# Optimization experiments

Measured on AMD Instinct MI355X. Metric: run time of the kernel, lower is better.

The kernel has to match this reference:

```python
import jax, jax.numpy as jnp
import numpy as np

ALL_OFFSETS = np.array([1, 3, 4, 13, 15, 21, 23, 28, 48, 64, 96, 192, 384, 512, 768, 1024], dtype=np.int32)
NEG_BIG = -1e30  # finite stand-in for -inf (avoids nan grads)


def setup_inputs() -> dict:
    key = jax.random.key(0)
    k0, k1, k2, k3, k4 = jax.random.split(key, 5)
    B, H, N, HD = 1, 16, 4096, 64
    return {
        "q": jax.random.normal(k0, (B, H, N, HD), dtype=jnp.float32),
        "k": jax.random.normal(k1, (B, H, N, HD), dtype=jnp.float32),
        "v": jax.random.normal(k2, (B, H, N, HD), dtype=jnp.float32),
        "pos_bias": jax.random.normal(k3, (16, H), dtype=jnp.float32) * 0.1,
        "scale_embed": jax.random.normal(k4, (16, HD), dtype=jnp.float32) * 0.1,
    }


def reference(q, k, v, pos_bias, scale_embed):
    # q,k,v: [B,H,N,HD]; pos_bias: [16,H]; scale_embed: [16,HD]
    B, H, N, HD = q.shape
    sc = 1.0 / np.sqrt(HD).astype(np.float32)
    offs = jnp.asarray(ALL_OFFSETS)                      # [16]
    idx = jnp.arange(N)[None, :] - offs[:, None]         # [16,N] key position n-delta
    valid = idx >= 0                                     # [16,N]
    idx_c = jnp.maximum(idx, 0)

    kg = k[:, :, idx_c, :]                               # [B,H,16,N,HD] gathered keys
    vg = v[:, :, idx_c, :]                               # [B,H,16,N,HD] gathered values

    # score = q.k/sqrt(HD) + pos_bias[i,h] + q.se_i/sqrt(HD)
    s = jnp.einsum('bhnd,bhind->bhin', q, kg) * sc
    s = s + pos_bias.T[None, :, :, None]                 # [H,16] -> broadcast over b,n
    s = s + jnp.einsum('bhnd,id->bhin', q, scale_embed) * sc
    s = jnp.where(valid[None, None], s, NEG_BIG)         # [B,H,16,N]

    # stable softmax over the 16 offsets; rows with no valid offset (n=0) yield 0 output
    m = jnp.max(s, axis=2, keepdims=True)                # [B,H,1,N]
    p = jnp.where(valid[None, None], jnp.exp(s - m), 0.0)  # [B,H,16,N]
    l = jnp.sum(p, axis=2)                               # [B,H,N]
    out = jnp.einsum('bhin,bhind->bhnd', p, vg)
    out = out / jnp.where(l > 0.0, l, 1.0)[..., None]
    return out
```

## Files before the change

kernel.cpp:

```cpp
#include <hip/hip_runtime.h>
#include <hip/hip_fp16.h>

typedef __attribute__((address_space(3))) float* lds_f32p;
typedef const __attribute__((address_space(1))) float* glob_f32p;

template<int CTRL>
__device__ __forceinline__ float dpp_add_step(float x) {
    const int p = __builtin_amdgcn_update_dpp(
        0, __builtin_bit_cast(int, x), CTRL, 0xf, 0xf, true);
    return x + __builtin_bit_cast(float, p);
}

__device__ __forceinline__ float dpp_reduce16(float a) {
    a = dpp_add_step<0xB1>(a);
    a = dpp_add_step<0x4E>(a);
    a = dpp_add_step<0x141>(a);
    a = dpp_add_step<0x140>(a);
    return a;
}

__device__ __forceinline__ float4 lds_h4(const __half* p) {
    const __half2* hp = (const __half2*)p;
    const float2 lo = __half22float2(hp[0]);
    const float2 hi = __half22float2(hp[1]);
    return make_float4(lo.x, lo.y, hi.x, hi.y);
}

template<bool SAFE>
__device__ __forceinline__ void run_block(
    const float* __restrict__ kh, const float* __restrict__ vh,
    const float* se_sh, const float* pb2,
    const __half* ksh, const __half* vsh,
    const float4 qa, const float4 qb, const int n0, const int n1,
    const int g, const int jo,
    float4& oa, float4& ob, float& la, float& lb)
{
    constexpr int NEARO[8] = {1, 3, 4, 13, 15, 21, 23, 28};
    constexpr int FARO[8]  = {48, 64, 96, 192, 384, 512, 768, 1024};
    constexpr float SC = 0.125f * 1.44269504f;

#pragma unroll
    for (int t = 0; t < 8; ++t) {
        {
            const int off = FARO[t];
            const int i = t + 8;
            const int ia = n0 - off, ib = n1 - off;
            const int iac = SAFE ? (ia < 0 ? 0 : ia) : ia;
            const int ibc = SAFE ? (ib < 0 ? 0 : ib) : ib;
            const float4 sv = *(const float4*)&se_sh[(i << 6) + jo];
            const float4 ka = *(const float4*)(kh + ((size_t)iac << 6) + jo);
            const float4 kb = *(const float4*)(kh + ((size_t)ibc << 6) + jo);
            const float4 va = *(const float4*)(vh + ((size_t)iac << 6) + jo);
            const float4 vb = *(const float4*)(vh + ((size_t)ibc << 6) + jo);
            float accA = qa.x*(ka.x+sv.x) + qa.y*(ka.y+sv.y) + qa.z*(ka.z+sv.z) + qa.w*(ka.w+sv.w);
            float accB = qb.x*(kb.x+sv.x) + qb.y*(kb.y+sv.y) + qb.z*(kb.z+sv.z) + qb.w*(kb.w+sv.w);
            accA = dpp_reduce16(accA);
            accB = dpp_reduce16(accB);
            float pA = exp2f(fmaf(accA, SC, pb2[i]));
            float pB = exp2f(fmaf(accB, SC, pb2[i]));
            if (SAFE) {
                pA = (ia >= 0) ? pA : 0.f;
                pB = (ib >= 0) ? pB : 0.f;
            }
            la += pA; lb += pB;
            oa.x += pA*va.x; oa.y += pA*va.y; oa.z += pA*va.z; oa.w += pA*va.w;
            ob.x += pB*vb.x; ob.y += pB*vb.y; ob.z += pB*vb.z; ob.w += pB*vb.w;
        }
        {
            const int off = NEARO[t];
            const int i = t;
            const int ia = n0 - off, ib = n1 - off;
            const float4 sv = *(const float4*)&se_sh[(i << 6) + jo];
            const float4 ka = lds_h4(&ksh[((g + 32 - off) << 6) + jo]);
            const float4 kb = lds_h4(&ksh[((g + 48 - off) << 6) + jo]);
            const float4 va = lds_h4(&vsh[((g + 32 - off) << 6) + jo]);
            const float4 vb = lds_h4(&vsh[((g + 48 - off) << 6) + jo]);
            float accA = qa.x*(ka.x+sv.x) + qa.y*(ka.y+sv.y) + qa.z*(ka.z+sv.z) + qa.w*(ka.w+sv.w);
            float accB = qb.x*(kb.x+sv.x) + qb.y*(kb.y+sv.y) + qb.z*(kb.z+sv.z) + qb.w*(kb.w+sv.w);
            accA = dpp_reduce16(accA);
            accB = dpp_reduce16(accB);
            float pA = exp2f(fmaf(accA, SC, pb2[i]));
            float pB = exp2f(fmaf(accB, SC, pb2[i]));
            if (SAFE) {
                pA = (ia >= 0) ? pA : 0.f;
                pB = (ib >= 0) ? pB : 0.f;
            }
            la += pA; lb += pB;
            oa.x += pA*va.x; oa.y += pA*va.y; oa.z += pA*va.z; oa.w += pA*va.w;
            ob.x += pB*vb.x; ob.y += pB*vb.y; ob.z += pB*vb.z; ob.w += pB*vb.w;
        }
    }
}

__global__ __launch_bounds__(256) void dsqg_attn_kernel(
    const float* __restrict__ q, const float* __restrict__ k,
    const float* __restrict__ v, const float* __restrict__ pb,
    const float* __restrict__ se, float* __restrict__ out)
{
    __shared__ __half ksh[64 * 64];
    __shared__ __half vsh[64 * 64];
    __shared__ float se_sh[16 * 64];

    const int p   = blockIdx.x;
    const int lb_ = ((p & 7) << 8) + (p >> 3);
    const int h   = lb_ >> 7;
    const int nb  = lb_ & 127;
    const int base = nb << 5;

    const int g  = threadIdx.x >> 4;
    const int j  = threadIdx.x & 15;
    const int n0 = base + g;
    const int n1 = n0 + 16;
    const size_t hb = (size_t)h << 18;
    const int jo = j << 2;

    const float* kh = k + hb;
    const float* vh = v + hb;

    {
        const float* src = se + (threadIdx.x << 2);
        float* dstbase = &se_sh[(threadIdx.x >> 6) << 8];
        __builtin_amdgcn_global_load_lds((glob_f32p)src, (lds_f32p)dstbase, 16, 0, 0);
    }

    const float4 qa = *(const float4*)(q + hb + ((size_t)n0 << 6) + jo);
    const float4 qb = *(const float4*)(q + hb + ((size_t)n1 << 6) + jo);

    {
        const int wave = threadIdx.x >> 6;
        const int lane = threadIdx.x & 63;
        const int srow = lane >> 4;
        const int scol = (lane & 15) << 2;
#pragma unroll
        for (int i = 0; i < 4; ++i) {
            const int sr = (wave << 4) + (i << 2) + srow;
            int gr = base - 32 + sr;
            gr = gr < 0 ? 0 : gr;
            const size_t go = ((size_t)gr << 6) + scol;
            const float4 kf = *(const float4*)(kh + go);
            const float4 vf = *(const float4*)(vh + go);
            union { __half2 h2[2]; uint2 u; } pk, pv;
            pk.h2[0] = __floats2half2_rn(kf.x, kf.y);
            pk.h2[1] = __floats2half2_rn(kf.z, kf.w);
            pv.h2[0] = __floats2half2_rn(vf.x, vf.y);
            pv.h2[1] = __floats2half2_rn(vf.z, vf.w);
            *(uint2*)&ksh[(sr << 6) + scol] = pk.u;
            *(uint2*)&vsh[(sr << 6) + scol] = pv.u;
        }
    }

    float pb2[16];
#pragma unroll
    for (int i = 0; i < 16; ++i) pb2[i] = pb[(i << 4) + h] * 1.44269504f;

    __syncthreads();

    float la = 0.f, lb2 = 0.f;
    float4 oa = make_float4(0.f, 0.f, 0.f, 0.f);
    float4 ob = make_float4(0.f, 0.f, 0.f, 0.f);

    if (nb >= 32) {
        run_block<false>(kh, vh, se_sh, pb2, ksh, vsh, qa, qb, n0, n1, g, jo, oa, ob, la, lb2);
    } else {
        run_block<true>(kh, vh, se_sh, pb2, ksh, vsh, qa, qb, n0, n1, g, jo, oa, ob, la, lb2);
    }

    const float inva = (la > 0.f) ? 1.f / la : 0.f;
    const float invb = 1.f / lb2;
    oa.x *= inva; oa.y *= inva; oa.z *= inva; oa.w *= inva;
    ob.x *= invb; ob.y *= invb; ob.z *= invb; ob.w *= invb;
    *(float4*)(out + hb + ((size_t)n0 << 6) + jo) = oa;
    *(float4*)(out + hb + ((size_t)n1 << 6) + jo) = ob;
}

extern "C" void kernel_launch(void* const* d_in, const int* in_sizes, int n_in,
                              void* d_out, int out_size, void* d_ws, size_t ws_size,
                              hipStream_t stream) {
    const float* q  = (const float*)d_in[0];
    const float* k  = (const float*)d_in[1];
    const float* v  = (const float*)d_in[2];
    const float* pb = (const float*)d_in[3];
    const float* se = (const float*)d_in[4];
    float* out = (float*)d_out;

    dim3 grid(2048);
    dim3 block(256);
    dsqg_attn_kernel<<<grid, block, 0, stream>>>(q, k, v, pb, se, out);
}
```

Before: 25.38 us.

## Remap threads to 8 lanes per query and precompute scale-embed bias terms

Each query row is now handled by 8 lanes holding 8 dims each, instead of 16 lanes handling two rows with 4 dims each. This shortens the cross-lane DPP reduction to 3 steps and allows 128-bit LDS and global loads. The q·scale_embed term is hoisted out of the per-offset loop into 16 precomputed per-row biases, which removes the add of se to k inside the inner loop. Scale_embed is now staged through LDS as fp16 via a plain register copy instead of global_load_lds, which slightly reduces the precision of the bias.

Result: no change. 24.93 us (-1.8%).

```diff
diff --git a/kernel.cpp b/kernel.cpp
--- a/kernel.cpp
+++ b/kernel.cpp
@@ -1,8 +1,5 @@
 #include <hip/hip_runtime.h>
 #include <hip/hip_fp16.h>
-
-typedef __attribute__((address_space(3))) float* lds_f32p;
-typedef const __attribute__((address_space(1))) float* glob_f32p;
 
 template<int CTRL>
 __device__ __forceinline__ float dpp_add_step(float x) {
@@ -11,29 +8,36 @@
     return x + __builtin_bit_cast(float, p);
 }
 
-__device__ __forceinline__ float dpp_reduce16(float a) {
+__device__ __forceinline__ float dpp_reduce8(float a) {
     a = dpp_add_step<0xB1>(a);
     a = dpp_add_step<0x4E>(a);
     a = dpp_add_step<0x141>(a);
-    a = dpp_add_step<0x140>(a);
     return a;
 }
 
-__device__ __forceinline__ float4 lds_h4(const __half* p) {
-    const __half2* hp = (const __half2*)p;
-    const float2 lo = __half22float2(hp[0]);
-    const float2 hi = __half22float2(hp[1]);
-    return make_float4(lo.x, lo.y, hi.x, hi.y);
+__device__ __forceinline__ void lds_h8(const __half* p, float4& a, float4& b) {
+    const uint4 u = *(const uint4*)p;
+    const float2 f0 = __half22float2(__builtin_bit_cast(__half2, u.x));
+    const float2 f1 = __half22float2(__builtin_bit_cast(__half2, u.y));
+    const float2 f2 = __half22float2(__builtin_bit_cast(__half2, u.z));
+    const float2 f3 = __half22float2(__builtin_bit_cast(__half2, u.w));
+    a = make_float4(f0.x, f0.y, f1.x, f1.y);
+    b = make_float4(f2.x, f2.y, f3.x, f3.y);
+}
+
+__device__ __forceinline__ float dot8(const float4 q0, const float4 q1,
+                                      const float4 a, const float4 b) {
+    return q0.x*a.x + q0.y*a.y + q0.z*a.z + q0.w*a.w
+         + q1.x*b.x + q1.y*b.y + q1.z*b.z + q1.w*b.w;
 }
 
 template<bool SAFE>
 __device__ __forceinline__ void run_block(
     const float* __restrict__ kh, const float* __restrict__ vh,
-    const float* se_sh, const float* pb2,
+    const float* bias,
     const __half* ksh, const __half* vsh,
-    const float4 qa, const float4 qb, const int n0, const int n1,
-    const int g, const int jo,
-    float4& oa, float4& ob, float& la, float& lb)
+    const float4 q0, const float4 q1, const int n, const int ql, const int d8,
+    float4& o0, float4& o1, float& l)
 {
     constexpr int NEARO[8] = {1, 3, 4, 13, 15, 21, 23, 28};
     constexpr int FARO[8]  = {48, 64, 96, 192, 384, 512, 768, 1024};
@@ -42,52 +46,34 @@
 #pragma unroll
     for (int t = 0; t < 8; ++t) {
         {
-            const int off = FARO[t];
-            const int i = t + 8;
-            const int ia = n0 - off, ib = n1 - off;
-            const int iac = SAFE ? (ia < 0 ? 0 : ia) : ia;
-            const int ibc = SAFE ? (ib < 0 ? 0 : ib) : ib;
-            const float4 sv = *(const float4*)&se_sh[(i << 6) + jo];
-            const float4 ka = *(const float4*)(kh + ((size_t)iac << 6) + jo);
-            const float4 kb = *(const float4*)(kh + ((size_t)ibc << 6) + jo);
-            const float4 va = *(const float4*)(vh + ((size_t)iac << 6) + jo);
-            const float4 vb = *(const float4*)(vh + ((size_t)ibc << 6) + jo);
-            float accA = qa.x*(ka.x+sv.x) + qa.y*(ka.y+sv.y) + qa.z*(ka.z+sv.z) + qa.w*(ka.w+sv.w);
-            float accB = qb.x*(kb.x+sv.x) + qb.y*(kb.y+sv.y) + qb.z*(kb.z+sv.z) + qb.w*(kb.w+sv.w);
-            accA = dpp_reduce16(accA);
-            accB = dpp_reduce16(accB);
-            float pA = exp2f(fmaf(accA, SC, pb2[i]));
-            float pB = exp2f(fmaf(accB, SC, pb2[i]));
-            if (SAFE) {
-                pA = (ia >= 0) ? pA : 0.f;
-                pB = (ib >= 0) ? pB : 0.f;
-            }
-            la += pA; lb += pB;
-            oa.x += pA*va.x; oa.y += pA*va.y; oa.z += pA*va.z; oa.w += pA*va.w;
-            ob.x += pB*vb.x; ob.y += pB*vb.y; ob.z += pB*vb.z; ob.w += pB*vb.w;
+            const int off  = FARO[t];
+            const int idx  = n - off;
+            const int idxc = SAFE ? (idx < 0 ? 0 : idx) : idx;
+            const float4* kp = (const float4*)(kh + ((size_t)idxc << 6) + d8);
+            const float4 k0 = kp[0], k1 = kp[1];
+            const float4* vp = (const float4*)(vh + ((size_t)idxc << 6) + d8);
+            const float4 v0 = vp[0], v1 = vp[1];
+            float a = dot8(q0, q1, k0, k1);
+            a = dpp_reduce8(a);
+            float pw = exp2f(fmaf(a, SC, bias[t + 8]));
+            if (SAFE) pw = (idx >= 0) ? pw : 0.f;
+            l += pw;
+            o0.x += pw*v0.x; o0.y += pw*v0.y; o0.z += pw*v0.z; o0.w += pw*v0.w;
+            o1.x += pw*v1.x; o1.y += pw*v1.y; o1.z += pw*v1.z; o1.w += pw*v1.w;
         }
         {
             const int off = NEARO[t];
-            const int i = t;
-            const int ia = n0 - off, ib = n1 - off;
-            const float4 sv = *(const float4*)&se_sh[(i << 6) + jo];
-            const float4 ka = lds_h4(&ksh[((g + 32 - off) << 6) + jo]);
-            const float4 kb = lds_h4(&ksh[((g + 48 - off) << 6) + jo]);
-            const float4 va = lds_h4(&vsh[((g + 32 - off) << 6) + jo]);
-            const float4 vb = lds_h4(&vsh[((g + 48 - off) << 6) + jo]);
-            float accA = qa.x*(ka.x+sv.x) + qa.y*(ka.y+sv.y) + qa.z*(ka.z+sv.z) + qa.w*(ka.w+sv.w);
-            float accB = qb.x*(kb.x+sv.x) + qb.y*(kb.y+sv.y) + qb.z*(kb.z+sv.z) + qb.w*(kb.w+sv.w);
-            accA = dpp_reduce16(accA);
-            accB = dpp_reduce16(accB);
-            float pA = exp2f(fmaf(accA, SC, pb2[i]));
-            float pB = exp2f(fmaf(accB, SC, pb2[i]));
-            if (SAFE) {
-                pA = (ia >= 0) ? pA : 0.f;
-                pB = (ib >= 0) ? pB : 0.f;
-            }
-            la += pA; lb += pB;
-            oa.x += pA*va.x; oa.y += pA*va.y; oa.z += pA*va.z; oa.w += pA*va.w;
-            ob.x += pB*vb.x; ob.y += pB*vb.y; ob.z += pB*vb.z; ob.w += pB*vb.w;
+            const int row = ql + 32 - off;
+            float4 k0, k1, v0, v1;
+            lds_h8(&ksh[(row << 6) + d8], k0, k1);
+            lds_h8(&vsh[(row << 6) + d8], v0, v1);
+            float a = dot8(q0, q1, k0, k1);
+            a = dpp_reduce8(a);
+            float pw = exp2f(fmaf(a, SC, bias[t]));
+            if (SAFE) pw = (n - off >= 0) ? pw : 0.f;
+            l += pw;
+            o0.x += pw*v0.x; o0.y += pw*v0.y; o0.z += pw*v0.z; o0.w += pw*v0.w;
+            o1.x += pw*v1.x; o1.y += pw*v1.y; o1.z += pw*v1.z; o1.w += pw*v1.w;
         }
     }
 }
@@ -99,7 +85,7 @@
 {
     __shared__ __half ksh[64 * 64];
     __shared__ __half vsh[64 * 64];
-    __shared__ float se_sh[16 * 64];
+    __shared__ __half se_sh[16 * 64];
 
     const int p   = blockIdx.x;
     const int lb_ = ((p & 7) << 8) + (p >> 3);
@@ -107,24 +93,19 @@
     const int nb  = lb_ & 127;
     const int base = nb << 5;
 
-    const int g  = threadIdx.x >> 4;
-    const int j  = threadIdx.x & 15;
-    const int n0 = base + g;
-    const int n1 = n0 + 16;
+    const int g   = threadIdx.x >> 4;
+    const int j   = threadIdx.x & 15;
+    const int sub = j >> 3;
+    const int d8  = (j & 7) << 3;
+    const int ql  = (g << 1) + sub;
+    const int n   = base + ql;
     const size_t hb = (size_t)h << 18;
-    const int jo = j << 2;
 
     const float* kh = k + hb;
     const float* vh = v + hb;
 
-    {
-        const float* src = se + (threadIdx.x << 2);
-        float* dstbase = &se_sh[(threadIdx.x >> 6) << 8];
-        __builtin_amdgcn_global_load_lds((glob_f32p)src, (lds_f32p)dstbase, 16, 0, 0);
-    }
-
-    const float4 qa = *(const float4*)(q + hb + ((size_t)n0 << 6) + jo);
-    const float4 qb = *(const float4*)(q + hb + ((size_t)n1 << 6) + jo);
+    const float4* qp = (const float4*)(q + hb + ((size_t)n << 6) + d8);
+    const float4 q0 = qp[0], q1 = qp[1];
 
     {
         const int wave = threadIdx.x >> 6;
@@ -148,29 +129,42 @@
             *(uint2*)&vsh[(sr << 6) + scol] = pv.u;
         }
     }
-
-    float pb2[16];
-#pragma unroll
-    for (int i = 0; i < 16; ++i) pb2[i] = pb[(i << 4) + h] * 1.44269504f;
+    {
+        const float4 sf = *(const float4*)(se + (threadIdx.x << 2));
+        union { __half2 h2[2]; uint2 u; } ps;
+        ps.h2[0] = __floats2half2_rn(sf.x, sf.y);
+        ps.h2[1] = __floats2half2_rn(sf.z, sf.w);
+        *(uint2*)&se_sh[threadIdx.x << 2] = ps.u;
+    }
 
     __syncthreads();
 
-    float la = 0.f, lb2 = 0.f;
-    float4 oa = make_float4(0.f, 0.f, 0.f, 0.f);
-    float4 ob = make_float4(0.f, 0.f, 0.f, 0.f);
+    constexpr float SC = 0.125f * 1.44269504f;
+    float bias[16];
+#pragma unroll
+    for (int i = 0; i < 16; ++i) {
+        float4 e0, e1;
+        lds_h8(&se_sh[(i << 6) + d8], e0, e1);
+        float a = dot8(q0, q1, e0, e1);
+        a = dpp_reduce8(a);
+        bias[i] = fmaf(a, SC, pb[(i << 4) + h] * 1.44269504f);
+    }
+
+    float l = 0.f;
+    float4 o0 = make_float4(0.f, 0.f, 0.f, 0.f);
+    float4 o1 = make_float4(0.f, 0.f, 0.f, 0.f);
 
     if (nb >= 32) {
-        run_block<false>(kh, vh, se_sh, pb2, ksh, vsh, qa, qb, n0, n1, g, jo, oa, ob, la, lb2);
+        run_block<false>(kh, vh, bias, ksh, vsh, q0, q1, n, ql, d8, o0, o1, l);
     } else {
-        run_block<true>(kh, vh, se_sh, pb2, ksh, vsh, qa, qb, n0, n1, g, jo, oa, ob, la, lb2);
+        run_block<true>(kh, vh, bias, ksh, vsh, q0, q1, n, ql, d8, o0, o1, l);
     }
 
-    const float inva = (la > 0.f) ? 1.f / la : 0.f;
-    const float invb = 1.f / lb2;
-    oa.x *= inva; oa.y *= inva; oa.z *= inva; oa.w *= inva;
-    ob.x *= invb; ob.y *= invb; ob.z *= invb; ob.w *= invb;
-    *(float4*)(out + hb + ((size_t)n0 << 6) + jo) = oa;
-    *(float4*)(out + hb + ((size_t)n1 << 6) + jo) = ob;
+    const float inv = (l > 0.f) ? 1.f / l : 0.f;
+    o0.x *= inv; o0.y *= inv; o0.z *= inv; o0.w *= inv;
+    o1.x *= inv; o1.y *= inv; o1.z *= inv; o1.w *= inv;
+    float4* op = (float4*)(out + hb + ((size_t)n << 6) + d8);
+    op[0] = o0; op[1] = o1;
 }
 
 extern "C" void kernel_launch(void* const* d_in, const int* in_sizes, int n_in,
```
